# Optimization experiments

Hardware: AMD Instinct MI355X
Metric: run time of the kernel (lower is better)

Reference implementation:

```python
import jax, jax.numpy as jnp
import numpy as np

DIM = 512
NUM_GROUPS = 32
NUM_HEADS = 8
EPS = 1e-5


def group_norm(x, gamma, beta):
    # x: (B, C, H, W); normalize over (C//G, H, W) per group
    B, C, H, W = x.shape
    g = x.reshape(B, NUM_GROUPS, -1)
    mean = g.mean(axis=2, keepdims=True)
    var = g.var(axis=2, keepdims=True)
    g = (g - mean) * jax.lax.rsqrt(var + EPS)
    x = g.reshape(B, C, H, W)
    return x * gamma[None, :, None, None] + beta[None, :, None, None]


def setup_inputs() -> dict:
    key = jax.random.key(0)
    ks = jax.random.split(key, 7)
    B, C, H, W = 16, DIM, 32, 32
    x = jax.random.normal(ks[0], (B, C, H, W), dtype=jnp.float32)
    gamma = jnp.ones((C,), dtype=jnp.float32)
    beta = jnp.zeros((C,), dtype=jnp.float32)
    s_in = 1.0 / np.sqrt(C)
    w_qkv = jax.random.normal(ks[1], (3 * C, C), dtype=jnp.float32) * s_in
    b_qkv = jnp.zeros((3 * C,), dtype=jnp.float32)
    w_proj = jax.random.normal(ks[2], (C, C), dtype=jnp.float32) * s_in
    b_proj = jnp.zeros((C,), dtype=jnp.float32)
    return {"x": x, "gamma": gamma, "beta": beta, "w_qkv": w_qkv,
            "b_qkv": b_qkv, "w_proj": w_proj, "b_proj": b_proj}


def reference(x, gamma, beta, w_qkv, b_qkv, w_proj, b_proj):
    B, C, H, W = x.shape
    nh = NUM_HEADS
    c3 = 3 * C // nh          # per-head qkv channels (3 * head_dim)
    dh = C // nh              # head_dim
    scale = C ** (-0.5)       # NOTE: source scales by full dim, not head_dim

    h = group_norm(x, gamma, beta)

    # 1x1 conv qkv projection: (B, 3C, H, W)
    qkv = jnp.einsum('bchw,oc->bohw', h, w_qkv) + b_qkv[None, :, None, None]

    # rearrange 'b (head c) h w -> (b head) (h w) c'
    qkv = qkv.reshape(B, nh, c3, H, W)
    qkv = qkv.transpose(0, 1, 3, 4, 2).reshape(B * nh, H * W, c3)
    q, k, v = jnp.split(qkv, 3, axis=2)   # each (B*nh, HW, dh)

    score = jnp.einsum('bnc,bmc->bnm', q, k * scale)   # (B*nh, HW, HW)
    attn = jax.nn.softmax(score, axis=2)
    out = jnp.einsum('bnm,bmc->bnc', attn, v)          # (B*nh, HW, dh)

    # rearrange '(head b) (h w) c -> b (head c) h w'  (NOTE head-major, as in source)
    out = out.reshape(nh, B, H, W, dh)
    out = out.transpose(1, 0, 4, 2, 3).reshape(B, C, H, W)

    out = jnp.einsum('bchw,oc->bohw', out, w_proj) + b_proj[None, :, None, None]
    return out + x
```

## Files before the change

### kernel.cpp

```cpp
#include <hip/hip_runtime.h>
#include <stdint.h>

typedef __bf16 bf16;
typedef __attribute__((ext_vector_type(4))) float f32x4;
typedef __attribute__((ext_vector_type(8))) __bf16 bf16x8;
typedef __attribute__((ext_vector_type(4))) __bf16 bf16x4;

#define NB 16
#define CH 512
#define HWS 1024
#define NHEAD 8
#define DH 64
#define O3 1536
#define NG 32
#define LDP 72

__global__ void gn_stats(const float* __restrict__ x, float* __restrict__ stats) {
    int bg = blockIdx.x;
    int b = bg >> 5, g = bg & 31;
    const float4* p = (const float4*)(x + ((size_t)(b * CH + g * 16)) * HWS);
    float s = 0.f, ss = 0.f;
    for (int i = threadIdx.x; i < 4096; i += 256) {
        float4 v = p[i];
        s  += v.x + v.y + v.z + v.w;
        ss += v.x*v.x + v.y*v.y + v.z*v.z + v.w*v.w;
    }
    for (int off = 32; off; off >>= 1) {
        s  += __shfl_xor(s,  off, 64);
        ss += __shfl_xor(ss, off, 64);
    }
    __shared__ float red[8];
    int w = threadIdx.x >> 6;
    if ((threadIdx.x & 63) == 0) { red[w*2] = s; red[w*2+1] = ss; }
    __syncthreads();
    if (threadIdx.x == 0) {
        float S  = red[0] + red[2] + red[4] + red[6];
        float SS = red[1] + red[3] + red[5] + red[7];
        float mean = S * (1.f/16384.f);
        float var  = SS * (1.f/16384.f) - mean*mean;
        stats[bg*2]   = mean;
        stats[bg*2+1] = rsqrtf(var + 1e-5f);
    }
}

__global__ void cvt_w(const float* __restrict__ wq, const float* __restrict__ wp,
                      bf16* __restrict__ wq_b, bf16* __restrict__ wp_b) {
    int i = blockIdx.x * 256 + threadIdx.x;
    if (i < O3*CH) wq_b[i] = (bf16)wq[i];
    else           wp_b[i - O3*CH] = (bf16)wp[i - O3*CH];
}

__global__ void gn_apply_t(const float* __restrict__ x, const float* __restrict__ stats,
                           const float* __restrict__ gamma, const float* __restrict__ beta,
                           bf16* __restrict__ hT) {
    __shared__ float tile[32][33];
    int bx = blockIdx.x;
    int b = bx >> 9;
    int rem = bx & 511;
    int ct = rem >> 5, nt = rem & 31;
    int tx = threadIdx.x & 31, ty = threadIdx.x >> 5;
    #pragma unroll
    for (int r = 0; r < 4; ++r) {
        int c = ct*32 + ty + r*8;
        int n = nt*32 + tx;
        float v = x[((size_t)(b * CH + c)) * HWS + n];
        int g = c >> 4;
        float mean = stats[(b*32+g)*2], rstd = stats[(b*32+g)*2+1];
        tile[ty + r*8][tx] = (v - mean) * rstd * gamma[c] + beta[c];
    }
    __syncthreads();
    #pragma unroll
    for (int r = 0; r < 4; ++r) {
        int n = nt*32 + ty + r*8;
        int c = ct*32 + tx;
        hT[((size_t)(b * HWS + n)) * CH + c] = (bf16)tile[tx][ty + r*8];
    }
}

__global__ __launch_bounds__(256, 3)
void qkv_gemm(const bf16* __restrict__ W, const bf16* __restrict__ hT,
              const float* __restrict__ bias, bf16* __restrict__ qkv) {
    __shared__ __align__(16) bf16 As[128*LDP];
    __shared__ __align__(16) bf16 Bs[128*LDP];
    int bx = blockIdx.x;
    int po = bx >> 7, qo = bx & 127;
    int obase = po*128, bnbase = qo*128;
    int tid = threadIdx.x;
    int lane = tid & 63, w = tid >> 6;
    int quad = lane >> 4, l15 = lane & 15;
    int wm = w >> 1, wn = w & 1;

    f32x4 acc[4][4] = {};
    for (int k0 = 0; k0 < 512; k0 += 64) {
        #pragma unroll
        for (int r = 0; r < 4; ++r) {
            int c = r*256 + tid;
            int row = c >> 3, dc = c & 7;
            uint4 va = *(const uint4*)(W  + ((size_t)(obase + row)) * 512 + k0 + dc*8);
            *(uint4*)(&As[row*LDP + dc*8]) = va;
            uint4 vb = *(const uint4*)(hT + ((size_t)(bnbase + row)) * 512 + k0 + dc*8);
            *(uint4*)(&Bs[row*LDP + dc*8]) = vb;
        }
        __syncthreads();
        #pragma unroll
        for (int ks = 0; ks < 2; ++ks) {
            bf16x8 af[4], bfv[4];
            #pragma unroll
            for (int mt = 0; mt < 4; ++mt)
                af[mt] = *(const bf16x8*)(&As[(wm*64 + mt*16 + l15)*LDP + ks*32 + quad*8]);
            #pragma unroll
            for (int nt = 0; nt < 4; ++nt)
                bfv[nt] = *(const bf16x8*)(&Bs[(wn*64 + nt*16 + l15)*LDP + ks*32 + quad*8]);
            #pragma unroll
            for (int mt = 0; mt < 4; ++mt)
                #pragma unroll
                for (int nt = 0; nt < 4; ++nt)
                    acc[mt][nt] = __builtin_amdgcn_mfma_f32_16x16x32_bf16(af[mt], bfv[nt], acc[mt][nt], 0, 0, 0);
        }
        __syncthreads();
    }
    #pragma unroll
    for (int mt = 0; mt < 4; ++mt) {
        int o0 = obase + wm*64 + mt*16 + quad*4;
        float4 bb = *(const float4*)(bias + o0);
        #pragma unroll
        for (int nt = 0; nt < 4; ++nt) {
            int bn = bnbase + wn*64 + nt*16 + l15;
            bf16x4 v;
            v[0] = (bf16)(acc[mt][nt][0] + bb.x);
            v[1] = (bf16)(acc[mt][nt][1] + bb.y);
            v[2] = (bf16)(acc[mt][nt][2] + bb.z);
            v[3] = (bf16)(acc[mt][nt][3] + bb.w);
            *(bf16x4*)(qkv + (size_t)bn * O3 + o0) = v;
        }
    }
}

__global__ void v_transpose(const bf16* __restrict__ qkv, bf16* __restrict__ vT) {
    __shared__ bf16 t[32][34];
    int bx = blockIdx.x;
    int g = bx >> 6;
    int rem = bx & 63;
    int dt = rem >> 5, kt = rem & 31;
    int b = g >> 3, h = g & 7;
    int tx = threadIdx.x & 31, ty = threadIdx.x >> 5;
    #pragma unroll
    for (int r = 0; r < 4; ++r) {
        int key = kt*32 + ty + r*8;
        int d = dt*32 + tx;
        t[ty + r*8][tx] = qkv[((size_t)(b * HWS + key)) * O3 + h*192 + 128 + d];
    }
    __syncthreads();
    #pragma unroll
    for (int r = 0; r < 4; ++r) {
        int d = dt*32 + ty + r*8;
        int key = kt*32 + tx;
        vT[((size_t)(g * DH + d)) * HWS + key] = t[tx][ty + r*8];
    }
}

__global__ __launch_bounds__(256, 4)
void flash_attn(const bf16* __restrict__ qkv, const bf16* __restrict__ vT,
                bf16* __restrict__ A2) {
    __shared__ __align__(16) bf16 Ks[64*LDP];
    __shared__ __align__(16) bf16 Vs[64*LDP];
    __shared__ __align__(16) bf16 Ps[4][32*LDP];
    int bx = blockIdx.x;
    int g = bx & 127, qt = bx >> 7;
    int b = g >> 3, h = g & 7;
    int tid = threadIdx.x, lane = tid & 63, w = tid >> 6;
    int quad = lane >> 4, l15 = lane & 15;
    const float kLog2 = 0.04419417382415922f * 1.44269504088896341f;

    bf16x8 aq[2][2];
    #pragma unroll
    for (int mt = 0; mt < 2; ++mt) {
        int qrow = qt*128 + w*32 + mt*16 + l15;
        const bf16* qb = qkv + ((size_t)(b * HWS + qrow)) * O3 + h*192;
        aq[mt][0] = *(const bf16x8*)(qb + quad*8);
        aq[mt][1] = *(const bf16x8*)(qb + 32 + quad*8);
    }

    f32x4 acc[2][4] = {};
    float L[2] = {0.f, 0.f};

    int r0 = tid >> 3, d0 = (tid & 7) * 8;
    int r1 = r0 + 32;
    const bf16* kp0 = qkv + ((size_t)(b * HWS + r0)) * O3 + h*192 + 64 + d0;
    const bf16* kp1 = qkv + ((size_t)(b * HWS + r1)) * O3 + h*192 + 64 + d0;
    const bf16* vp0 = vT + ((size_t)(g * DH + r0)) * HWS + d0;
    const bf16* vp1 = vT + ((size_t)(g * DH + r1)) * HWS + d0;
    bf16* ksd0 = &Ks[r0*LDP + d0];
    bf16* ksd1 = &Ks[r1*LDP + d0];
    bf16* vsd0 = &Vs[r0*LDP + d0];
    bf16* vsd1 = &Vs[r1*LDP + d0];

    uint4 ka = *(const uint4*)(kp0);
    uint4 kb = *(const uint4*)(kp1);
    uint4 va = *(const uint4*)(vp0);
    uint4 vb = *(const uint4*)(vp1);

    for (int kt = 0; kt < 16; ++kt) {
        __syncthreads();
        *(uint4*)ksd0 = ka;
        *(uint4*)ksd1 = kb;
        *(uint4*)vsd0 = va;
        *(uint4*)vsd1 = vb;
        __syncthreads();
        if (kt < 15) {
            size_t ko = (size_t)(kt+1) * 64 * O3;
            size_t vo = (size_t)(kt+1) * 64;
            ka = *(const uint4*)(kp0 + ko);
            kb = *(const uint4*)(kp1 + ko);
            va = *(const uint4*)(vp0 + vo);
            vb = *(const uint4*)(vp1 + vo);
        }

        #pragma unroll
        for (int nt = 0; nt < 4; ++nt) {
            bf16x8 ak0 = *(const bf16x8*)(&Ks[(nt*16 + l15)*LDP + quad*8]);
            bf16x8 ak1 = *(const bf16x8*)(&Ks[(nt*16 + l15)*LDP + 32 + quad*8]);
            #pragma unroll
            for (int mt = 0; mt < 2; ++mt) {
                f32x4 z = {};
                z = __builtin_amdgcn_mfma_f32_16x16x32_bf16(ak0, aq[mt][0], z, 0, 0, 0);
                z = __builtin_amdgcn_mfma_f32_16x16x32_bf16(ak1, aq[mt][1], z, 0, 0, 0);
                bf16x4 p;
                #pragma unroll
                for (int r = 0; r < 4; ++r) {
                    float e = exp2f(z[r] * kLog2);
                    L[mt] += e;
                    p[r] = (bf16)e;
                }
                *(bf16x4*)(&Ps[w][(mt*16 + l15)*LDP + nt*16 + quad*4]) = p;
            }
        }
        bf16x8 ap[2][2];
        #pragma unroll
        for (int mt = 0; mt < 2; ++mt) {
            ap[mt][0] = *(const bf16x8*)(&Ps[w][(mt*16 + l15)*LDP + quad*8]);
            ap[mt][1] = *(const bf16x8*)(&Ps[w][(mt*16 + l15)*LDP + 32 + quad*8]);
        }
        #pragma unroll
        for (int dt = 0; dt < 4; ++dt) {
            bf16x8 bv0 = *(const bf16x8*)(&Vs[(dt*16 + l15)*LDP + quad*8]);
            bf16x8 bv1 = *(const bf16x8*)(&Vs[(dt*16 + l15)*LDP + 32 + quad*8]);
            #pragma unroll
            for (int mt = 0; mt < 2; ++mt) {
                acc[mt][dt] = __builtin_amdgcn_mfma_f32_16x16x32_bf16(ap[mt][0], bv0, acc[mt][dt], 0, 0, 0);
                acc[mt][dt] = __builtin_amdgcn_mfma_f32_16x16x32_bf16(ap[mt][1], bv1, acc[mt][dt], 0, 0, 0);
            }
        }
    }

    float Linv[2][4];
    #pragma unroll
    for (int mt = 0; mt < 2; ++mt) {
        float Lf = L[mt];
        Lf += __shfl_xor(Lf, 16, 64);
        Lf += __shfl_xor(Lf, 32, 64);
        #pragma unroll
        for (int r = 0; r < 4; ++r)
            Linv[mt][r] = 1.f / __shfl(Lf, quad*4 + r, 64);
    }

    __syncthreads();
    #pragma unroll
    for (int mt = 0; mt < 2; ++mt)
        #pragma unroll
        for (int dt = 0; dt < 4; ++dt)
            #pragma unroll
            for (int r = 0; r < 4; ++r)
                Ps[w][(mt*16 + quad*4 + r)*LDP + dt*16 + l15] = (bf16)(acc[mt][dt][r] * Linv[mt][r]);

    int bp = g & 15;
    int hp = g >> 4;
    #pragma unroll
    for (int cc = 0; cc < 4; ++cc) {
        int c = cc*64 + lane;
        int row = c >> 3, dc = c & 7;
        uint4 v = *(const uint4*)(&Ps[w][row*LDP + dc*8]);
        size_t idx = ((size_t)(bp * HWS + qt*128 + w*32 + row)) * CH + hp*64 + dc*8;
        *(uint4*)(A2 + idx) = v;
    }
}

__global__ __launch_bounds__(256, 3)
void proj_gemm(const bf16* __restrict__ A2, const bf16* __restrict__ Wp,
               const float* __restrict__ bias, const float* __restrict__ x,
               float* __restrict__ out) {
    __shared__ __align__(16) bf16 As[128*LDP];
    __shared__ __align__(16) bf16 Bs[128*LDP];
    int bx = blockIdx.x;
    int po = bx >> 7, qo = bx & 127;
    int obase = po*128, bnbase = qo*128;
    int tid = threadIdx.x;
    int lane = tid & 63, w = tid >> 6;
    int quad = lane >> 4, l15 = lane & 15;
    int wm = w >> 1, wn = w & 1;

    f32x4 acc[4][4] = {};
    for (int k0 = 0; k0 < 512; k0 += 64) {
        #pragma unroll
        for (int r = 0; r < 4; ++r) {
            int c = r*256 + tid;
            int row = c >> 3, dc = c & 7;
            uint4 va = *(const uint4*)(A2 + ((size_t)(bnbase + row)) * 512 + k0 + dc*8);
            *(uint4*)(&As[row*LDP + dc*8]) = va;
            uint4 vb = *(const uint4*)(Wp + ((size_t)(obase + row)) * 512 + k0 + dc*8);
            *(uint4*)(&Bs[row*LDP + dc*8]) = vb;
        }
        __syncthreads();
        #pragma unroll
        for (int ks = 0; ks < 2; ++ks) {
            bf16x8 af[4], bfv[4];
            #pragma unroll
            for (int mt = 0; mt < 4; ++mt)
                af[mt] = *(const bf16x8*)(&As[(wm*64 + mt*16 + l15)*LDP + ks*32 + quad*8]);
            #pragma unroll
            for (int nt = 0; nt < 4; ++nt)
                bfv[nt] = *(const bf16x8*)(&Bs[(wn*64 + nt*16 + l15)*LDP + ks*32 + quad*8]);
            #pragma unroll
            for (int mt = 0; mt < 4; ++mt)
                #pragma unroll
                for (int nt = 0; nt < 4; ++nt)
                    acc[mt][nt] = __builtin_amdgcn_mfma_f32_16x16x32_bf16(af[mt], bfv[nt], acc[mt][nt], 0, 0, 0);
        }
        __syncthreads();
    }
    #pragma unroll
    for (int mt = 0; mt < 4; ++mt) {
        int bn0 = bnbase + wm*64 + mt*16 + quad*4;
        int bb = bn0 >> 10, n = bn0 & 1023;
        #pragma unroll
        for (int nt = 0; nt < 4; ++nt) {
            int o = obase + wn*64 + nt*16 + l15;
            size_t idx = ((size_t)(bb * CH + o)) * HWS + n;
            float4 xr = *(const float4*)(x + idx);
            float bv = bias[o];
            float4 res;
            res.x = acc[mt][nt][0] + bv + xr.x;
            res.y = acc[mt][nt][1] + bv + xr.y;
            res.z = acc[mt][nt][2] + bv + xr.z;
            res.w = acc[mt][nt][3] + bv + xr.w;
            *(float4*)(out + idx) = res;
        }
    }
}

extern "C" void kernel_launch(void* const* d_in, const int* in_sizes, int n_in,
                              void* d_out, int out_size, void* d_ws, size_t ws_size,
                              hipStream_t stream) {
    const float* x      = (const float*)d_in[0];
    const float* gamma  = (const float*)d_in[1];
    const float* beta   = (const float*)d_in[2];
    const float* w_qkv  = (const float*)d_in[3];
    const float* b_qkv  = (const float*)d_in[4];
    const float* w_proj = (const float*)d_in[5];
    const float* b_proj = (const float*)d_in[6];
    float* out = (float*)d_out;

    char* ws = (char*)d_ws;
    float* stats = (float*)(ws + 0);
    bf16*  wq_b  = (bf16*)(ws + 4096);
    bf16*  wp_b  = (bf16*)(ws + 1576960);
    bf16*  hT    = (bf16*)(ws + 2101248);
    bf16*  qkv   = (bf16*)(ws + 18878464);
    bf16*  vT    = (bf16*)(ws + 69210112);
    bf16*  A2    = hT;

    gn_stats   <<<512,  256, 0, stream>>>(x, stats);
    cvt_w      <<<4096, 256, 0, stream>>>(w_qkv, w_proj, wq_b, wp_b);
    gn_apply_t <<<8192, 256, 0, stream>>>(x, stats, gamma, beta, hT);
    qkv_gemm   <<<1536, 256, 0, stream>>>(wq_b, hT, b_qkv, qkv);
    v_transpose<<<8192, 256, 0, stream>>>(qkv, vT);
    flash_attn <<<1024, 256, 0, stream>>>(qkv, vT, A2);
    proj_gemm  <<<512,  256, 0, stream>>>(A2, wp_b, b_proj, x, out);
}
```

Baseline: 243.3 us.

## Fuse prep kernels, fold V transpose into QKV GEMM epilogue, stage proj epilogue

Measured after the change: 220.2 us. 9.5% less time.

```diff
diff --git a/kernel.cpp b/kernel.cpp
--- a/kernel.cpp
+++ b/kernel.cpp
@@ -12,42 +12,44 @@
 #define NHEAD 8
 #define DH 64
 #define O3 1536
-#define NG 32
 #define LDP 72
-
-__global__ void gn_stats(const float* __restrict__ x, float* __restrict__ stats) {
-    int bg = blockIdx.x;
-    int b = bg >> 5, g = bg & 31;
-    const float4* p = (const float4*)(x + ((size_t)(b * CH + g * 16)) * HWS);
-    float s = 0.f, ss = 0.f;
-    for (int i = threadIdx.x; i < 4096; i += 256) {
-        float4 v = p[i];
-        s  += v.x + v.y + v.z + v.w;
-        ss += v.x*v.x + v.y*v.y + v.z*v.z + v.w*v.w;
-    }
-    for (int off = 32; off; off >>= 1) {
-        s  += __shfl_xor(s,  off, 64);
-        ss += __shfl_xor(ss, off, 64);
-    }
-    __shared__ float red[8];
-    int w = threadIdx.x >> 6;
-    if ((threadIdx.x & 63) == 0) { red[w*2] = s; red[w*2+1] = ss; }
-    __syncthreads();
-    if (threadIdx.x == 0) {
-        float S  = red[0] + red[2] + red[4] + red[6];
-        float SS = red[1] + red[3] + red[5] + red[7];
-        float mean = S * (1.f/16384.f);
-        float var  = SS * (1.f/16384.f) - mean*mean;
-        stats[bg*2]   = mean;
-        stats[bg*2+1] = rsqrtf(var + 1e-5f);
-    }
-}
-
-__global__ void cvt_w(const float* __restrict__ wq, const float* __restrict__ wp,
-                      bf16* __restrict__ wq_b, bf16* __restrict__ wp_b) {
-    int i = blockIdx.x * 256 + threadIdx.x;
-    if (i < O3*CH) wq_b[i] = (bf16)wq[i];
-    else           wp_b[i - O3*CH] = (bf16)wp[i - O3*CH];
+#define CPQ 136
+#define CPF 132
+
+__global__ void prep(const float* __restrict__ x, float* __restrict__ stats,
+                     const float* __restrict__ wq, const float* __restrict__ wp,
+                     bf16* __restrict__ wq_b, bf16* __restrict__ wp_b) {
+    int bx = blockIdx.x;
+    if (bx < 512) {
+        int b = bx >> 5, g = bx & 31;
+        const float4* p = (const float4*)(x + ((size_t)(b * CH + g * 16)) * HWS);
+        float s = 0.f, ss = 0.f;
+        for (int i = threadIdx.x; i < 4096; i += 256) {
+            float4 v = p[i];
+            s  += v.x + v.y + v.z + v.w;
+            ss += v.x*v.x + v.y*v.y + v.z*v.z + v.w*v.w;
+        }
+        for (int off = 32; off; off >>= 1) {
+            s  += __shfl_xor(s,  off, 64);
+            ss += __shfl_xor(ss, off, 64);
+        }
+        __shared__ float red[8];
+        int w = threadIdx.x >> 6;
+        if ((threadIdx.x & 63) == 0) { red[w*2] = s; red[w*2+1] = ss; }
+        __syncthreads();
+        if (threadIdx.x == 0) {
+            float S  = red[0] + red[2] + red[4] + red[6];
+            float SS = red[1] + red[3] + red[5] + red[7];
+            float mean = S * (1.f/16384.f);
+            float var  = SS * (1.f/16384.f) - mean*mean;
+            stats[bx*2]   = mean;
+            stats[bx*2+1] = rsqrtf(var + 1e-5f);
+        }
+    } else {
+        int i = (bx - 512) * 256 + threadIdx.x;
+        if (i < O3*CH) wq_b[i] = (bf16)wq[i];
+        else           wp_b[i - O3*CH] = (bf16)wp[i - O3*CH];
+    }
 }
 
 __global__ void gn_apply_t(const float* __restrict__ x, const float* __restrict__ stats,
@@ -79,9 +81,11 @@
 
 __global__ __launch_bounds__(256, 3)
 void qkv_gemm(const bf16* __restrict__ W, const bf16* __restrict__ hT,
-              const float* __restrict__ bias, bf16* __restrict__ qkv) {
-    __shared__ __align__(16) bf16 As[128*LDP];
-    __shared__ __align__(16) bf16 Bs[128*LDP];
+              const float* __restrict__ bias, bf16* __restrict__ qkv,
+              bf16* __restrict__ vT) {
+    __shared__ __align__(16) bf16 SMEM[2*128*LDP];
+    bf16* As = SMEM;
+    bf16* Bs = SMEM + 128*LDP;
     int bx = blockIdx.x;
     int po = bx >> 7, qo = bx & 127;
     int obase = po*128, bnbase = qo*128;
@@ -119,43 +123,46 @@
         }
         __syncthreads();
     }
+
+    bf16* Cs = SMEM;
+    int b = bnbase >> 10;
+    int nbase = bnbase & 1023;
     #pragma unroll
     for (int mt = 0; mt < 4; ++mt) {
         int o0 = obase + wm*64 + mt*16 + quad*4;
         float4 bb = *(const float4*)(bias + o0);
+        int c192 = o0 % 192;
+        bool isV = (c192 >= 128);
+        int h = o0 / 192;
+        int d0 = c192 - 128;
         #pragma unroll
         for (int nt = 0; nt < 4; ++nt) {
-            int bn = bnbase + wn*64 + nt*16 + l15;
+            int bn_l = wn*64 + nt*16 + l15;
             bf16x4 v;
             v[0] = (bf16)(acc[mt][nt][0] + bb.x);
             v[1] = (bf16)(acc[mt][nt][1] + bb.y);
             v[2] = (bf16)(acc[mt][nt][2] + bb.z);
             v[3] = (bf16)(acc[mt][nt][3] + bb.w);
-            *(bf16x4*)(qkv + (size_t)bn * O3 + o0) = v;
-        }
-    }
-}
-
-__global__ void v_transpose(const bf16* __restrict__ qkv, bf16* __restrict__ vT) {
-    __shared__ bf16 t[32][34];
-    int bx = blockIdx.x;
-    int g = bx >> 6;
-    int rem = bx & 63;
-    int dt = rem >> 5, kt = rem & 31;
-    int b = g >> 3, h = g & 7;
-    int tx = threadIdx.x & 31, ty = threadIdx.x >> 5;
-    #pragma unroll
-    for (int r = 0; r < 4; ++r) {
-        int key = kt*32 + ty + r*8;
-        int d = dt*32 + tx;
-        t[ty + r*8][tx] = qkv[((size_t)(b * HWS + key)) * O3 + h*192 + 128 + d];
+            *(bf16x4*)(&Cs[bn_l*CPQ + (o0 - obase)]) = v;
+            if (isV) {
+                int key = nbase + bn_l;
+                size_t vb_ = ((size_t)((b*8 + h)*64 + d0)) * HWS + key;
+                vT[vb_]          = v[0];
+                vT[vb_ + HWS]    = v[1];
+                vT[vb_ + 2*HWS]  = v[2];
+                vT[vb_ + 3*HWS]  = v[3];
+            }
+        }
     }
     __syncthreads();
     #pragma unroll
-    for (int r = 0; r < 4; ++r) {
-        int d = dt*32 + ty + r*8;
-        int key = kt*32 + tx;
-        vT[((size_t)(g * DH + d)) * HWS + key] = t[tx][ty + r*8];
+    for (int p = 0; p < 8; ++p) {
+        int bn_l = p*16 + (tid >> 4);
+        int o8 = (tid & 15) * 8;
+        if ((obase + o8) % 192 < 128) {
+            uint4 v = *(const uint4*)(&Cs[bn_l*CPQ + o8]);
+            *(uint4*)(qkv + ((size_t)(bnbase + bn_l)) * O3 + obase + o8) = v;
+        }
     }
 }
 
@@ -289,8 +296,9 @@
 void proj_gemm(const bf16* __restrict__ A2, const bf16* __restrict__ Wp,
                const float* __restrict__ bias, const float* __restrict__ x,
                float* __restrict__ out) {
-    __shared__ __align__(16) bf16 As[128*LDP];
-    __shared__ __align__(16) bf16 Bs[128*LDP];
+    __shared__ __align__(16) bf16 SMEM[2*128*LDP];
+    bf16* As = SMEM;
+    bf16* Bs = SMEM + 128*LDP;
     int bx = blockIdx.x;
     int po = bx >> 7, qo = bx & 127;
     int obase = po*128, bnbase = qo*128;
@@ -328,23 +336,42 @@
         }
         __syncthreads();
     }
-    #pragma unroll
-    for (int mt = 0; mt < 4; ++mt) {
-        int bn0 = bnbase + wm*64 + mt*16 + quad*4;
-        int bb = bn0 >> 10, n = bn0 & 1023;
-        #pragma unroll
-        for (int nt = 0; nt < 4; ++nt) {
-            int o = obase + wn*64 + nt*16 + l15;
-            size_t idx = ((size_t)(bb * CH + o)) * HWS + n;
-            float4 xr = *(const float4*)(x + idx);
+
+    float* Cf = (float*)SMEM;
+    int bb = bnbase >> 10;
+    int nbase = bnbase & 1023;
+    #pragma unroll
+    for (int hh = 0; hh < 2; ++hh) {
+        if (wm == hh) {
+            #pragma unroll
+            for (int mt = 0; mt < 4; ++mt)
+                #pragma unroll
+                for (int nt = 0; nt < 4; ++nt)
+                    #pragma unroll
+                    for (int r = 0; r < 4; ++r)
+                        Cf[(mt*16 + quad*4 + r)*CPF + wn*64 + nt*16 + l15] = acc[mt][nt][r];
+        }
+        __syncthreads();
+        #pragma unroll
+        for (int p = 0; p < 4; ++p) {
+            int ol = p*32 + (tid >> 3);
+            int nl0 = (tid & 7) * 8;
+            int o = obase + ol;
             float bv = bias[o];
-            float4 res;
-            res.x = acc[mt][nt][0] + bv + xr.x;
-            res.y = acc[mt][nt][1] + bv + xr.y;
-            res.z = acc[mt][nt][2] + bv + xr.z;
-            res.w = acc[mt][nt][3] + bv + xr.w;
-            *(float4*)(out + idx) = res;
-        }
+            #pragma unroll
+            for (int jj = 0; jj < 2; ++jj) {
+                int nl = nl0 + jj*4;
+                size_t idx = ((size_t)(bb * CH + o)) * HWS + nbase + hh*64 + nl;
+                float4 xr = *(const float4*)(x + idx);
+                float4 res;
+                res.x = Cf[(nl+0)*CPF + ol] + bv + xr.x;
+                res.y = Cf[(nl+1)*CPF + ol] + bv + xr.y;
+                res.z = Cf[(nl+2)*CPF + ol] + bv + xr.z;
+                res.w = Cf[(nl+3)*CPF + ol] + bv + xr.w;
+                *(float4*)(out + idx) = res;
+            }
+        }
+        __syncthreads();
     }
 }
 
@@ -369,11 +396,9 @@
     bf16*  vT    = (bf16*)(ws + 69210112);
     bf16*  A2    = hT;
 
-    gn_stats   <<<512,  256, 0, stream>>>(x, stats);
-    cvt_w      <<<4096, 256, 0, stream>>>(w_qkv, w_proj, wq_b, wp_b);
+    prep       <<<4608, 256, 0, stream>>>(x, stats, w_qkv, w_proj, wq_b, wp_b);
     gn_apply_t <<<8192, 256, 0, stream>>>(x, stats, gamma, beta, hT);
-    qkv_gemm   <<<1536, 256, 0, stream>>>(wq_b, hT, b_qkv, qkv);
-    v_transpose<<<8192, 256, 0, stream>>>(qkv, vT);
+    qkv_gemm   <<<1536, 256, 0, stream>>>(wq_b, hT, b_qkv, qkv, vT);
     flash_attn <<<1024, 256, 0, stream>>>(qkv, vT, A2);
     proj_gemm  <<<512,  256, 0, stream>>>(A2, wp_b, b_proj, x, out);
 }
```
